# Kernel optimization log

Hardware: AMD Instinct MI355X
Metric: run time of the kernel (lower is better)

The kernel has to match this reference:

```python
import jax, jax.numpy as jnp
import numpy as np

B, S, D, DOUT, E = 2, 2048, 1024, 1024, 8
DH = 4 * D  # expert hidden size


def setup_inputs() -> dict:
    key = jax.random.key(0)
    ks = jax.random.split(key, 7)
    sc = lambda *sh: 1.0 / np.sqrt(sh[-2]) if len(sh) >= 2 else 0.02
    return {
        "x": jax.random.normal(ks[0], (B, S, D), jnp.float32),
        "Wg": jax.random.normal(ks[1], (D, E), jnp.float32) / np.sqrt(D),
        "bg": jnp.zeros((E,), jnp.float32),
        "W1": jax.random.normal(ks[2], (E, D, DH), jnp.float32) / np.sqrt(D),
        "b1": jax.random.normal(ks[3], (E, DH), jnp.float32) * 0.02,
        "W2": jax.random.normal(ks[4], (E, DH, DOUT), jnp.float32) / np.sqrt(DH),
        "b2": jax.random.normal(ks[5], (E, DOUT), jnp.float32) * 0.02,
    }


def reference(x, Wg, bg, W1, b1, W2, b2):
    # x: [B, S, D] -> flatten tokens (chunking over seq in the original is
    # math-neutral: routing and expert MLP are per-token).
    Bb, Ss, Dd = x.shape
    xt = x.reshape(-1, Dd)                       # [T, D]
    # Gate: softmax then argmax (top-1 routing, output NOT scaled by gate prob)
    gates = jax.nn.softmax(xt @ Wg + bg, axis=-1)  # [T, E]
    sel = jnp.argmax(gates, axis=-1)               # [T]
    nE = W1.shape[0]
    out = jnp.zeros((xt.shape[0], W2.shape[-1]), x.dtype)
    # Grouped expert MLP expressed as masked dense loop over the small fixed
    # expert count (jit-friendly; a fused gather-grouped-GEMM-scatter kernel
    # is the optimization target).
    for e in range(nE):
        h = jax.nn.gelu(xt @ W1[e] + b1[e], approximate=False)  # [T, 4D]
        ye = h @ W2[e] + b2[e]                                  # [T, DOUT]
        out = jnp.where((sel == e)[:, None], ye, out)
    return out.reshape(Bb, Ss, -1)
```

## Files before the change

kernel.cpp:

```cpp
#include <hip/hip_runtime.h>
#include <hip/hip_bf16.h>
#include <math.h>

#define T_TOK 4096
#define DIM   1024
#define NEXP  8
#define DHID  4096
#define NDOUT 1024
#define BM    128
#define MAXTILES 40

typedef short bf16x8 __attribute__((ext_vector_type(8)));
typedef float f32x4 __attribute__((ext_vector_type(4)));

__device__ __forceinline__ unsigned short f2bf(float f) {
  unsigned u = __float_as_uint(f);
  u += 0x7fffu + ((u >> 16) & 1u);
  return (unsigned short)(u >> 16);
}
__device__ __forceinline__ unsigned pack2bf(float a, float b) {
  return (unsigned)f2bf(a) | ((unsigned)f2bf(b) << 16);
}
__device__ __forceinline__ void gl_lds16(const void* g, void* l) {
  __builtin_amdgcn_global_load_lds(
      (const __attribute__((address_space(1))) void*)g,
      (__attribute__((address_space(3))) void*)l, 16, 0, 0);
}

__global__ __launch_bounds__(256)
void gate_kernel(const float* __restrict__ x, const float* __restrict__ Wg,
                 const float* __restrict__ bg, int* __restrict__ sel) {
  int lane = threadIdx.x & 63;
  int wid  = threadIdx.x >> 6;
  int t = blockIdx.x * 4 + wid;
  if (t >= T_TOK) return;
  const float* xr = x + (size_t)t * DIM;
  double acc[NEXP];
#pragma unroll
  for (int e = 0; e < NEXP; e++) acc[e] = 0.0;
  for (int j = 0; j < DIM / 64; j++) {
    int d = lane + j * 64;
    float xv = xr[d];
    const float4* wr = reinterpret_cast<const float4*>(Wg + (size_t)d * NEXP);
    float4 w0 = wr[0], w1 = wr[1];
    acc[0] += (double)xv * (double)w0.x;
    acc[1] += (double)xv * (double)w0.y;
    acc[2] += (double)xv * (double)w0.z;
    acc[3] += (double)xv * (double)w0.w;
    acc[4] += (double)xv * (double)w1.x;
    acc[5] += (double)xv * (double)w1.y;
    acc[6] += (double)xv * (double)w1.z;
    acc[7] += (double)xv * (double)w1.w;
  }
#pragma unroll
  for (int off = 32; off >= 1; off >>= 1) {
#pragma unroll
    for (int e = 0; e < NEXP; e++) acc[e] += __shfl_down(acc[e], off);
  }
  if (lane == 0) {
    double best = acc[0] + (double)bg[0];
    int bi = 0;
#pragma unroll
    for (int e = 1; e < NEXP; e++) {
      double v = acc[e] + (double)bg[e];
      if (v > best) { best = v; bi = e; }
    }
    sel[t] = bi;
  }
}

__global__ void zero_kernel(int* __restrict__ counts) {
  if (threadIdx.x < NEXP) counts[threadIdx.x] = 0;
}

__global__ void hist_kernel(const int* __restrict__ sel, int* __restrict__ counts) {
  __shared__ int lc[NEXP];
  if (threadIdx.x < NEXP) lc[threadIdx.x] = 0;
  __syncthreads();
  int t = blockIdx.x * 256 + threadIdx.x;
  atomicAdd(&lc[sel[t]], 1);
  __syncthreads();
  if (threadIdx.x < NEXP) atomicAdd(&counts[threadIdx.x], lc[threadIdx.x]);
}

__global__ void plan_kernel(const int* __restrict__ counts, int* __restrict__ base,
                            int* __restrict__ cursor, int* __restrict__ tileExpert,
                            int* __restrict__ tilePos, int* __restrict__ tileRows,
                            int* __restrict__ ntiles) {
  if (threadIdx.x == 0) {
    int acc = 0, nt = 0;
    for (int e = 0; e < NEXP; e++) {
      base[e] = acc; cursor[e] = acc;
      int c = counts[e];
      for (int j = 0; j < c; j += BM) {
        tileExpert[nt] = e;
        tilePos[nt]    = acc + j;
        int rem = c - j;
        tileRows[nt]   = rem < BM ? rem : BM;
        nt++;
      }
      acc += c;
    }
    *ntiles = nt;
  }
}

__global__ void scatter_kernel(const int* __restrict__ sel, int* __restrict__ cursor,
                               int* __restrict__ list) {
  __shared__ int lcnt[NEXP];
  __shared__ int lbase[NEXP];
  int tid = threadIdx.x;
  if (tid < NEXP) lcnt[tid] = 0;
  __syncthreads();
  int t = blockIdx.x * 256 + tid;
  int e = sel[t];
  int lpos = atomicAdd(&lcnt[e], 1);
  __syncthreads();
  if (tid < NEXP) lbase[tid] = atomicAdd(&cursor[tid], lcnt[tid]);
  __syncthreads();
  list[lbase[e] + lpos] = t;
}

__global__ __launch_bounds__(256)
void convert_x_kernel(const float* __restrict__ x, unsigned short* __restrict__ xbf) {
  int i = (blockIdx.x * 256 + threadIdx.x) * 8;
  float4 a = *(const float4*)(x + i);
  float4 b = *(const float4*)(x + i + 4);
  uint4 o;
  o.x = pack2bf(a.x, a.y); o.y = pack2bf(a.z, a.w);
  o.z = pack2bf(b.x, b.y); o.w = pack2bf(b.z, b.w);
  *(uint4*)(xbf + i) = o;
}

__global__ __launch_bounds__(256)
void transpose_tile_kernel(const float* __restrict__ in, unsigned short* __restrict__ out,
                           int K, int N) {
  int nb = blockIdx.x, kb = blockIdx.y, e = blockIdx.z;
  const float* inp = in + (size_t)e * K * N;
  __shared__ unsigned short lds[128][72];
  int tx = threadIdx.x;
  int kloc = tx >> 5;
  int n4   = (tx & 31) << 2;
#pragma unroll
  for (int p = 0; p < 8; p++) {
    int k = p * 8 + kloc;
    float4 v = *(const float4*)(inp + (size_t)(kb * 64 + k) * N + nb * 128 + n4);
    lds[n4 + 0][k] = f2bf(v.x);
    lds[n4 + 1][k] = f2bf(v.y);
    lds[n4 + 2][k] = f2bf(v.z);
    lds[n4 + 3][k] = f2bf(v.w);
  }
  __syncthreads();
  char* tile = (char*)(out + (((size_t)e * gridDim.x + nb) * gridDim.y + kb) * 8192);
  int r  = tx >> 1;
  int kc0 = (tx & 1) * 32;
#pragma unroll
  for (int c = 0; c < 4; c++) {
    int kc = kc0 + c * 8;
    uint4 v = *(const uint4*)&lds[r][kc];
    *(uint4*)(tile + r * 128 + ((2 * kc) ^ ((r & 7) << 4))) = v;
  }
}


__global__ __launch_bounds__(256)
void gemm1_kernel(const unsigned short* __restrict__ xbf, const unsigned short* __restrict__ W1T,
                  const float* __restrict__ b1, const int* __restrict__ list,
                  const int* __restrict__ tileExpert, const int* __restrict__ tilePos,
                  const int* __restrict__ tileRows, const int* __restrict__ ntiles,
                  unsigned short* __restrict__ HcT) {
  int tIdx = blockIdx.y;
  if (tIdx >= *ntiles) return;
  int e = tileExpert[tIdx], posBase = tilePos[tIdx], rows = tileRows[tIdx];
  int nb = blockIdx.x;

  __shared__ __align__(1024) char As[128 * 128];
  __shared__ __align__(1024) char Bs[128 * 128];

  const int tx = threadIdx.x, lane = tx & 63, w = tx >> 6;
  const int wm = w >> 1, wn = w & 1;
  const int rsub = lane >> 3;
  const int px = ((lane & 7) ^ rsub) << 4;

  const char* aS[4];
#pragma unroll
  for (int j = 0; j < 4; j++) {
    int r = w * 32 + j * 8 + rsub;
    int tok = list[posBase + (r < rows ? r : rows - 1)];
    aS[j] = (const char*)xbf + (size_t)tok * (DIM * 2) + px;
  }
  const char* bTile = (const char*)W1T + (((size_t)e * (DHID / 128) + nb) * (DIM / 64)) * 16384
                      + w * 4096 + lane * 16;

  f32x4 acc[4][4];
#pragma unroll
  for (int mf = 0; mf < 4; mf++)
#pragma unroll
    for (int nf = 0; nf < 4; nf++)
      acc[mf][nf] = f32x4{0.f, 0.f, 0.f, 0.f};

  const int NT = DIM / 64;
  for (int kt = 0; kt < NT; kt++) {
#pragma unroll
    for (int j = 0; j < 4; j++) {
      gl_lds16(aS[j] + kt * 128, &As[(w * 32 + j * 8) * 128]);
      gl_lds16(bTile + kt * 16384 + j * 1024, &Bs[w * 4096 + j * 1024]);
    }
    __syncthreads();
#pragma unroll
    for (int ks = 0; ks < 2; ks++) {
      int koff = (ks * 64 + (lane >> 4) * 16) ^ ((lane & 7) << 4);
      bf16x8 aF[4], bF[4];
#pragma unroll
      for (int mf = 0; mf < 4; mf++)
        aF[mf] = *(const bf16x8*)&As[(wm * 64 + mf * 16 + (lane & 15)) * 128 + koff];
#pragma unroll
      for (int nf = 0; nf < 4; nf++)
        bF[nf] = *(const bf16x8*)&Bs[(wn * 64 + nf * 16 + (lane & 15)) * 128 + koff];
#pragma unroll
      for (int mf = 0; mf < 4; mf++)
#pragma unroll
        for (int nf = 0; nf < 4; nf++)
          acc[mf][nf] = __builtin_amdgcn_mfma_f32_16x16x32_bf16(aF[mf], bF[nf], acc[mf][nf], 0, 0, 0);
    }
    __syncthreads();
  }

  const float* b1e = b1 + (size_t)e * DHID;
  char* hBase = (char*)(HcT + (size_t)tIdx * (DHID / 64) * 8192);
#pragma unroll
  for (int nf = 0; nf < 4; nf++) {
    int col = nb * 128 + wn * 64 + nf * 16 + (lane & 15);
    int kt2 = col >> 6;
    int colk2 = (col & 63) * 2;
    float bias = b1e[col];
    char* tile = hBase + (size_t)kt2 * 16384;
#pragma unroll
    for (int mf = 0; mf < 4; mf++) {
#pragma unroll
      for (int j = 0; j < 4; j++) {
        int r = wm * 64 + mf * 16 + ((lane >> 4) << 2) + j;
        float h = acc[mf][nf][j] + bias;
        float g = 0.5f * h * (1.0f + erff(h * 0.70710678118654752f));
        *(unsigned short*)(tile + r * 128 + (colk2 ^ ((r & 7) << 4))) = f2bf(g);
      }
    }
  }
}

__global__ __launch_bounds__(256)
void gemm2_kernel(const unsigned short* __restrict__ HcT, const unsigned short* __restrict__ W2T,
                  const float* __restrict__ b2, const int* __restrict__ tileExpert,
                  const int* __restrict__ tilePos, const int* __restrict__ tileRows,
                  const int* __restrict__ ntiles, float* __restrict__ Ppart) {
  int tIdx = blockIdx.y;
  if (tIdx >= *ntiles) return;
  int e = tileExpert[tIdx], posBase = tilePos[tIdx], rows = tileRows[tIdx];
  int nb = blockIdx.x;
  int zs = blockIdx.z;

  __shared__ __align__(1024) char As[128 * 128];
  __shared__ __align__(1024) char Bs[128 * 128];

  const int tx = threadIdx.x, lane = tx & 63, w = tx >> 6;
  const int wm = w >> 1, wn = w & 1;

  const char* aTile = (const char*)HcT + (size_t)tIdx * (DHID / 64) * 16384
                      + (size_t)zs * 32 * 16384 + w * 4096 + lane * 16;
  const char* bTile = (const char*)W2T + (((size_t)e * (NDOUT / 128) + nb) * (DHID / 64)) * 16384
                      + (size_t)zs * 32 * 16384 + w * 4096 + lane * 16;

  f32x4 acc[4][4];
#pragma unroll
  for (int mf = 0; mf < 4; mf++)
#pragma unroll
    for (int nf = 0; nf < 4; nf++)
      acc[mf][nf] = f32x4{0.f, 0.f, 0.f, 0.f};

  const int NT = 32;
  for (int kt = 0; kt < NT; kt++) {
#pragma unroll
    for (int j = 0; j < 4; j++) {
      gl_lds16(aTile + kt * 16384 + j * 1024, &As[w * 4096 + j * 1024]);
      gl_lds16(bTile + kt * 16384 + j * 1024, &Bs[w * 4096 + j * 1024]);
    }
    __syncthreads();
#pragma unroll
    for (int ks = 0; ks < 2; ks++) {
      int koff = (ks * 64 + (lane >> 4) * 16) ^ ((lane & 7) << 4);
      bf16x8 aF[4], bF[4];
#pragma unroll
      for (int mf = 0; mf < 4; mf++)
        aF[mf] = *(const bf16x8*)&As[(wm * 64 + mf * 16 + (lane & 15)) * 128 + koff];
#pragma unroll
      for (int nf = 0; nf < 4; nf++)
        bF[nf] = *(const bf16x8*)&Bs[(wn * 64 + nf * 16 + (lane & 15)) * 128 + koff];
#pragma unroll
      for (int mf = 0; mf < 4; mf++)
#pragma unroll
        for (int nf = 0; nf < 4; nf++)
          acc[mf][nf] = __builtin_amdgcn_mfma_f32_16x16x32_bf16(aF[mf], bF[nf], acc[mf][nf], 0, 0, 0);
    }
    __syncthreads();
  }

  const float* b2e = b2 + (size_t)e * NDOUT;
  float* P = Ppart + (size_t)zs * T_TOK * NDOUT;
#pragma unroll
  for (int nf = 0; nf < 4; nf++) {
    int col = nb * 128 + wn * 64 + nf * 16 + (lane & 15);
    float bias = (zs == 0) ? b2e[col] : 0.f;
#pragma unroll
    for (int mf = 0; mf < 4; mf++)
#pragma unroll
      for (int j = 0; j < 4; j++) {
        int rloc = wm * 64 + mf * 16 + ((lane >> 4) << 2) + j;
        if (rloc < rows)
          P[(size_t)(posBase + rloc) * NDOUT + col] = acc[mf][nf][j] + bias;
      }
  }
}

__global__ __launch_bounds__(256)
void reduce_kernel(const float* __restrict__ Ppart, const int* __restrict__ list,
                   float* __restrict__ out) {
  int pos = blockIdx.x;
  int tok = list[pos];
  int c = threadIdx.x * 4;
  float4 a = *(const float4*)(Ppart + (size_t)pos * NDOUT + c);
  float4 b = *(const float4*)(Ppart + (size_t)T_TOK * NDOUT + (size_t)pos * NDOUT + c);
  float4 o; o.x = a.x + b.x; o.y = a.y + b.y; o.z = a.z + b.z; o.w = a.w + b.w;
  *(float4*)(out + (size_t)tok * NDOUT + c) = o;
}

extern "C" void kernel_launch(void* const* d_in, const int* in_sizes, int n_in,
                              void* d_out, int out_size, void* d_ws, size_t ws_size,
                              hipStream_t stream) {
  const float* x  = (const float*)d_in[0];
  const float* Wg = (const float*)d_in[1];
  const float* bg = (const float*)d_in[2];
  const float* W1 = (const float*)d_in[3];
  const float* b1 = (const float*)d_in[4];
  const float* W2 = (const float*)d_in[5];
  const float* b2 = (const float*)d_in[6];
  float* out = (float*)d_out;

  char* ws = (char*)d_ws;
  int* sel        = (int*)(ws);
  int* counts     = (int*)(ws + 16384);
  int* base       = (int*)(ws + 16448);
  int* cursor     = (int*)(ws + 16512);
  int* ntiles     = (int*)(ws + 16576);
  int* tileExpert = (int*)(ws + 16640);
  int* tilePos    = (int*)(ws + 16832);
  int* tileRows   = (int*)(ws + 17024);
  int* list       = (int*)(ws + 17408);

  unsigned short* xbf = (unsigned short*)(ws + (1ull << 20));
  unsigned short* HcT = (unsigned short*)(ws + (10ull << 20));
  unsigned short* W1T = (unsigned short*)(ws + (52ull << 20));
  unsigned short* W2T = (unsigned short*)(ws + (116ull << 20));
  float* Ppart        = (float*)(ws + (52ull << 20));

  gate_kernel<<<T_TOK / 4, 256, 0, stream>>>(x, Wg, bg, sel);
  zero_kernel<<<1, 64, 0, stream>>>(counts);
  hist_kernel<<<T_TOK / 256, 256, 0, stream>>>(sel, counts);
  plan_kernel<<<1, 64, 0, stream>>>(counts, base, cursor, tileExpert, tilePos, tileRows, ntiles);
  scatter_kernel<<<T_TOK / 256, 256, 0, stream>>>(sel, cursor, list);

  convert_x_kernel<<<T_TOK * DIM / (256 * 8), 256, 0, stream>>>(x, xbf);
  transpose_tile_kernel<<<dim3(DHID / 128, DIM / 64, NEXP), 256, 0, stream>>>(W1, W1T, DIM, DHID);
  transpose_tile_kernel<<<dim3(NDOUT / 128, DHID / 64, NEXP), 256, 0, stream>>>(W2, W2T, DHID, NDOUT);

  gemm1_kernel<<<dim3(DHID / 128, MAXTILES), 256, 0, stream>>>(
      xbf, W1T, b1, list, tileExpert, tilePos, tileRows, ntiles, HcT);
  gemm2_kernel<<<dim3(NDOUT / 128, MAXTILES, 2), 256, 0, stream>>>(
      HcT, W2T, b2, tileExpert, tilePos, tileRows, ntiles, Ppart);
  reduce_kernel<<<T_TOK, 256, 0, stream>>>(Ppart, list, out);
}
```

Before: 307.5 us.

## Double-buffer LDS in expert GEMMs and fuse x bf16 conversion into gate

Both grouped GEMM kernels now use two LDS buffers. The next K tile is issued with async global-to-LDS loads while the current tile is computed, using an explicit vmcnt wait and raw barriers in place of two __syncthreads per iteration. Separately, the gate kernel now writes the bf16 copy of x while it reads x, which removes the standalone convert kernel and its second pass over x. LDS per block doubles to 64KB, which may lower occupancy, and the hand-written waitcnt depends on the exact count of outstanding loads.

```diff
diff --git a/kernel.cpp b/kernel.cpp
--- a/kernel.cpp
+++ b/kernel.cpp
@@ -26,31 +26,43 @@
       (const __attribute__((address_space(1))) void*)g,
       (__attribute__((address_space(3))) void*)l, 16, 0, 0);
 }
+#define SBAR()  __builtin_amdgcn_s_barrier()
+#define SCHED() __builtin_amdgcn_sched_barrier(0)
 
 __global__ __launch_bounds__(256)
 void gate_kernel(const float* __restrict__ x, const float* __restrict__ Wg,
-                 const float* __restrict__ bg, int* __restrict__ sel) {
+                 const float* __restrict__ bg, int* __restrict__ sel,
+                 unsigned short* __restrict__ xbf) {
   int lane = threadIdx.x & 63;
   int wid  = threadIdx.x >> 6;
   int t = blockIdx.x * 4 + wid;
   if (t >= T_TOK) return;
   const float* xr = x + (size_t)t * DIM;
+  unsigned short* xbr = xbf + (size_t)t * DIM;
   double acc[NEXP];
 #pragma unroll
   for (int e = 0; e < NEXP; e++) acc[e] = 0.0;
-  for (int j = 0; j < DIM / 64; j++) {
-    int d = lane + j * 64;
-    float xv = xr[d];
-    const float4* wr = reinterpret_cast<const float4*>(Wg + (size_t)d * NEXP);
-    float4 w0 = wr[0], w1 = wr[1];
-    acc[0] += (double)xv * (double)w0.x;
-    acc[1] += (double)xv * (double)w0.y;
-    acc[2] += (double)xv * (double)w0.z;
-    acc[3] += (double)xv * (double)w0.w;
-    acc[4] += (double)xv * (double)w1.x;
-    acc[5] += (double)xv * (double)w1.y;
-    acc[6] += (double)xv * (double)w1.z;
-    acc[7] += (double)xv * (double)w1.w;
+#pragma unroll
+  for (int j = 0; j < 4; j++) {
+    int d0 = j * 256 + lane * 4;
+    float4 v = *(const float4*)(xr + d0);
+    uint2 p; p.x = pack2bf(v.x, v.y); p.y = pack2bf(v.z, v.w);
+    *(uint2*)(xbr + d0) = p;
+    float xs[4] = {v.x, v.y, v.z, v.w};
+#pragma unroll
+    for (int i = 0; i < 4; i++) {
+      const float4* wr = reinterpret_cast<const float4*>(Wg + (size_t)(d0 + i) * NEXP);
+      float4 w0 = wr[0], w1 = wr[1];
+      double xv = (double)xs[i];
+      acc[0] += xv * (double)w0.x;
+      acc[1] += xv * (double)w0.y;
+      acc[2] += xv * (double)w0.z;
+      acc[3] += xv * (double)w0.w;
+      acc[4] += xv * (double)w1.x;
+      acc[5] += xv * (double)w1.y;
+      acc[6] += xv * (double)w1.z;
+      acc[7] += xv * (double)w1.w;
+    }
   }
 #pragma unroll
   for (int off = 32; off >= 1; off >>= 1) {
@@ -122,17 +134,6 @@
 }
 
 __global__ __launch_bounds__(256)
-void convert_x_kernel(const float* __restrict__ x, unsigned short* __restrict__ xbf) {
-  int i = (blockIdx.x * 256 + threadIdx.x) * 8;
-  float4 a = *(const float4*)(x + i);
-  float4 b = *(const float4*)(x + i + 4);
-  uint4 o;
-  o.x = pack2bf(a.x, a.y); o.y = pack2bf(a.z, a.w);
-  o.z = pack2bf(b.x, b.y); o.w = pack2bf(b.z, b.w);
-  *(uint4*)(xbf + i) = o;
-}
-
-__global__ __launch_bounds__(256)
 void transpose_tile_kernel(const float* __restrict__ in, unsigned short* __restrict__ out,
                            int K, int N) {
   int nb = blockIdx.x, kb = blockIdx.y, e = blockIdx.z;
@@ -174,8 +175,8 @@
   int e = tileExpert[tIdx], posBase = tilePos[tIdx], rows = tileRows[tIdx];
   int nb = blockIdx.x;
 
-  __shared__ __align__(1024) char As[128 * 128];
-  __shared__ __align__(1024) char Bs[128 * 128];
+  __shared__ __align__(1024) char As[2][16384];
+  __shared__ __align__(1024) char Bs[2][16384];
 
   const int tx = threadIdx.x, lane = tx & 63, w = tx >> 6;
   const int wm = w >> 1, wn = w & 1;
@@ -192,6 +193,14 @@
   const char* bTile = (const char*)W1T + (((size_t)e * (DHID / 128) + nb) * (DIM / 64)) * 16384
                       + w * 4096 + lane * 16;
 
+  auto STAGE = [&](int buf, int kt) {
+#pragma unroll
+    for (int j = 0; j < 4; j++) {
+      gl_lds16(aS[j] + kt * 128, &As[buf][(w * 32 + j * 8) * 128]);
+      gl_lds16(bTile + kt * 16384 + j * 1024, &Bs[buf][w * 4096 + j * 1024]);
+    }
+  };
+
   f32x4 acc[4][4];
 #pragma unroll
   for (int mf = 0; mf < 4; mf++)
@@ -199,31 +208,38 @@
     for (int nf = 0; nf < 4; nf++)
       acc[mf][nf] = f32x4{0.f, 0.f, 0.f, 0.f};
 
-  const int NT = DIM / 64;
-  for (int kt = 0; kt < NT; kt++) {
-#pragma unroll
-    for (int j = 0; j < 4; j++) {
-      gl_lds16(aS[j] + kt * 128, &As[(w * 32 + j * 8) * 128]);
-      gl_lds16(bTile + kt * 16384 + j * 1024, &Bs[w * 4096 + j * 1024]);
-    }
-    __syncthreads();
+  auto COMPUTE = [&](int buf) {
 #pragma unroll
     for (int ks = 0; ks < 2; ks++) {
       int koff = (ks * 64 + (lane >> 4) * 16) ^ ((lane & 7) << 4);
       bf16x8 aF[4], bF[4];
 #pragma unroll
       for (int mf = 0; mf < 4; mf++)
-        aF[mf] = *(const bf16x8*)&As[(wm * 64 + mf * 16 + (lane & 15)) * 128 + koff];
+        aF[mf] = *(const bf16x8*)&As[buf][(wm * 64 + mf * 16 + (lane & 15)) * 128 + koff];
 #pragma unroll
       for (int nf = 0; nf < 4; nf++)
-        bF[nf] = *(const bf16x8*)&Bs[(wn * 64 + nf * 16 + (lane & 15)) * 128 + koff];
+        bF[nf] = *(const bf16x8*)&Bs[buf][(wn * 64 + nf * 16 + (lane & 15)) * 128 + koff];
 #pragma unroll
       for (int mf = 0; mf < 4; mf++)
 #pragma unroll
         for (int nf = 0; nf < 4; nf++)
           acc[mf][nf] = __builtin_amdgcn_mfma_f32_16x16x32_bf16(aF[mf], bF[nf], acc[mf][nf], 0, 0, 0);
     }
-    __syncthreads();
+  };
+
+  const int NT = DIM / 64;
+  STAGE(0, 0);
+  for (int kt = 0; kt < NT; kt++) {
+    int buf = kt & 1;
+    if (kt + 1 < NT) {
+      STAGE(buf ^ 1, kt + 1);
+      asm volatile("s_waitcnt vmcnt(8)" ::: "memory");
+    } else {
+      asm volatile("s_waitcnt vmcnt(0)" ::: "memory");
+    }
+    SCHED(); SBAR(); SCHED();
+    COMPUTE(buf);
+    SCHED(); SBAR(); SCHED();
   }
 
   const float* b1e = b1 + (size_t)e * DHID;
@@ -259,8 +275,8 @@
   int nb = blockIdx.x;
   int zs = blockIdx.z;
 
-  __shared__ __align__(1024) char As[128 * 128];
-  __shared__ __align__(1024) char Bs[128 * 128];
+  __shared__ __align__(1024) char As[2][16384];
+  __shared__ __align__(1024) char Bs[2][16384];
 
   const int tx = threadIdx.x, lane = tx & 63, w = tx >> 6;
   const int wm = w >> 1, wn = w & 1;
@@ -270,6 +286,14 @@
   const char* bTile = (const char*)W2T + (((size_t)e * (NDOUT / 128) + nb) * (DHID / 64)) * 16384
                       + (size_t)zs * 32 * 16384 + w * 4096 + lane * 16;
 
+  auto STAGE = [&](int buf, int kt) {
+#pragma unroll
+    for (int j = 0; j < 4; j++) {
+      gl_lds16(aTile + kt * 16384 + j * 1024, &As[buf][w * 4096 + j * 1024]);
+      gl_lds16(bTile + kt * 16384 + j * 1024, &Bs[buf][w * 4096 + j * 1024]);
+    }
+  };
+
   f32x4 acc[4][4];
 #pragma unroll
   for (int mf = 0; mf < 4; mf++)
@@ -277,31 +301,38 @@
     for (int nf = 0; nf < 4; nf++)
       acc[mf][nf] = f32x4{0.f, 0.f, 0.f, 0.f};
 
-  const int NT = 32;
-  for (int kt = 0; kt < NT; kt++) {
-#pragma unroll
-    for (int j = 0; j < 4; j++) {
-      gl_lds16(aTile + kt * 16384 + j * 1024, &As[w * 4096 + j * 1024]);
-      gl_lds16(bTile + kt * 16384 + j * 1024, &Bs[w * 4096 + j * 1024]);
-    }
-    __syncthreads();
+  auto COMPUTE = [&](int buf) {
 #pragma unroll
     for (int ks = 0; ks < 2; ks++) {
       int koff = (ks * 64 + (lane >> 4) * 16) ^ ((lane & 7) << 4);
       bf16x8 aF[4], bF[4];
 #pragma unroll
       for (int mf = 0; mf < 4; mf++)
-        aF[mf] = *(const bf16x8*)&As[(wm * 64 + mf * 16 + (lane & 15)) * 128 + koff];
+        aF[mf] = *(const bf16x8*)&As[buf][(wm * 64 + mf * 16 + (lane & 15)) * 128 + koff];
 #pragma unroll
       for (int nf = 0; nf < 4; nf++)
-        bF[nf] = *(const bf16x8*)&Bs[(wn * 64 + nf * 16 + (lane & 15)) * 128 + koff];
+        bF[nf] = *(const bf16x8*)&Bs[buf][(wn * 64 + nf * 16 + (lane & 15)) * 128 + koff];
 #pragma unroll
       for (int mf = 0; mf < 4; mf++)
 #pragma unroll
         for (int nf = 0; nf < 4; nf++)
           acc[mf][nf] = __builtin_amdgcn_mfma_f32_16x16x32_bf16(aF[mf], bF[nf], acc[mf][nf], 0, 0, 0);
     }
-    __syncthreads();
+  };
+
+  const int NT = 32;
+  STAGE(0, 0);
+  for (int kt = 0; kt < NT; kt++) {
+    int buf = kt & 1;
+    if (kt + 1 < NT) {
+      STAGE(buf ^ 1, kt + 1);
+      asm volatile("s_waitcnt vmcnt(8)" ::: "memory");
+    } else {
+      asm volatile("s_waitcnt vmcnt(0)" ::: "memory");
+    }
+    SCHED(); SBAR(); SCHED();
+    COMPUTE(buf);
+    SCHED(); SBAR(); SCHED();
   }
 
   const float* b2e = b2 + (size_t)e * NDOUT;
@@ -362,13 +393,12 @@
   unsigned short* W2T = (unsigned short*)(ws + (116ull << 20));
   float* Ppart        = (float*)(ws + (52ull << 20));
 
-  gate_kernel<<<T_TOK / 4, 256, 0, stream>>>(x, Wg, bg, sel);
+  gate_kernel<<<T_TOK / 4, 256, 0, stream>>>(x, Wg, bg, sel, xbf);
   zero_kernel<<<1, 64, 0, stream>>>(counts);
   hist_kernel<<<T_TOK / 256, 256, 0, stream>>>(sel, counts);
   plan_kernel<<<1, 64, 0, stream>>>(counts, base, cursor, tileExpert, tilePos, tileRows, ntiles);
   scatter_kernel<<<T_TOK / 256, 256, 0, stream>>>(sel, cursor, list);
 
-  convert_x_kernel<<<T_TOK * DIM / (256 * 8), 256, 0, stream>>>(x, xbf);
   transpose_tile_kernel<<<dim3(DHID / 128, DIM / 64, NEXP), 256, 0, stream>>>(W1, W1T, DIM, DHID);
   transpose_tile_kernel<<<dim3(NDOUT / 128, DHID / 64, NEXP), 256, 0, stream>>>(W2, W2T, DHID, NDOUT);
 
```

Result: slower. 316.7 us (+3.0%).
